# Performance work log

Measured on AMD Instinct MI355X. Metric: run time of the kernel, lower is better.

Reference implementation:

```python
import jax, jax.numpy as jnp
import numpy as np

ALPHA = 1.702
LIMIT = 7.0


def setup_inputs() -> dict:
    key = jax.random.key(0)
    ks = jax.random.split(key, 7)
    B, S, H, D, E, TOPK = 2, 2048, 2048, 2048, 8, 4
    T = B * S
    hidden_states = jax.random.normal(ks[0], (B, S, H), dtype=jnp.float32)
    gate_up_proj = jax.random.normal(ks[1], (E, H, 2 * D), dtype=jnp.float32) * 0.02
    gate_up_proj_bias = jax.random.normal(ks[2], (E, 2 * D), dtype=jnp.float32) * 0.02
    down_proj = jax.random.normal(ks[3], (E, D, H), dtype=jnp.float32) * 0.02
    down_proj_bias = jax.random.normal(ks[4], (E, H), dtype=jnp.float32) * 0.02
    rw = jax.random.uniform(ks[5], (T, E), dtype=jnp.float32)
    routing_weights = rw / jnp.sum(rw, axis=-1, keepdims=True)
    router_indices = jax.random.randint(ks[6], (T, TOPK), 0, E, dtype=jnp.int64)
    return {
        "hidden_states": hidden_states,
        "gate_up_proj": gate_up_proj,
        "gate_up_proj_bias": gate_up_proj_bias,
        "down_proj": down_proj,
        "down_proj_bias": down_proj_bias,
        "routing_weights": routing_weights,
        "router_indices": router_indices,
    }


def geglu(gate_up):
    # interleaved layout: gate = [..., 0::2], up = [..., 1::2]
    gate = gate_up[..., 0::2]
    up = gate_up[..., 1::2]
    gate = jnp.minimum(gate, LIMIT)
    up = jnp.clip(up, -LIMIT, LIMIT)
    glu = gate * jax.nn.sigmoid(gate * ALPHA)
    return (up + 1.0) * glu


def reference(hidden_states, gate_up_proj, gate_up_proj_bias, down_proj,
              down_proj_bias, routing_weights, router_indices):
    B, S, H = hidden_states.shape
    x = hidden_states.reshape(-1, H)  # [T, H]
    # per-expert batched GEMM: [E, T, 2D]
    gate_up = jnp.einsum('th,ehd->etd', x, gate_up_proj) + gate_up_proj_bias[:, None, :]
    act = geglu(gate_up)  # [E, T, D]
    out = jnp.einsum('etd,edh->eth', act, down_proj) + down_proj_bias[:, None, :]
    # weight by router probs and sum over experts
    out = out * routing_weights.T[:, :, None]  # [E, T, H]
    out = jnp.sum(out, axis=0)
    return out.reshape(B, S, H)
```

## Files before the change

### kernel.cpp

```cpp
#include <hip/hip_runtime.h>
#include <hip/hip_bf16.h>

#define ALPHA 1.702f
#define GLIMIT 7.0f

typedef __attribute__((ext_vector_type(4))) float f32x4;
typedef __attribute__((ext_vector_type(8))) __bf16 bf16x8;

typedef __attribute__((address_space(3))) unsigned int as3_uint;
typedef const __attribute__((address_space(1))) unsigned int as1_uint;

__device__ __forceinline__ void async_copy16(void* lds, const void* g) {
    __builtin_amdgcn_global_load_lds((as1_uint*)g, (as3_uint*)lds, 16, 0, 0);
}

__device__ __forceinline__ short f2bf(float f) {
    unsigned u = __float_as_uint(f);
    unsigned r = (u + 0x7fffu + ((u >> 16) & 1u)) >> 16;
    return (short)r;
}

__global__ void cvt_bf16_kernel(const float* __restrict__ src,
                                short* __restrict__ dst, int n4) {
    int i = blockIdx.x * blockDim.x + threadIdx.x;
    if (i < n4) {
        float4 v = reinterpret_cast<const float4*>(src)[i];
        short4 o;
        o.x = f2bf(v.x); o.y = f2bf(v.y); o.z = f2bf(v.z); o.w = f2bf(v.w);
        reinterpret_cast<short4*>(dst)[i] = o;
    }
}

__global__ void transpose_cvt(const float* __restrict__ src,
                              short* __restrict__ dst, int R, int C) {
    __shared__ float t[64][65];
    const int z  = blockIdx.z;
    const int c0 = blockIdx.x * 64;
    const int r0 = blockIdx.y * 64;
    const float* s = src + (size_t)z * R * C;
    short* d = dst + (size_t)z * R * C;
    const int tid = threadIdx.x;
#pragma unroll
    for (int i = 0; i < 16; ++i) {
        int idx = i * 256 + tid;
        int r = idx >> 6, c = idx & 63;
        t[r][c] = s[(size_t)(r0 + r) * C + c0 + c];
    }
    __syncthreads();
#pragma unroll
    for (int i = 0; i < 16; ++i) {
        int idx = i * 256 + tid;
        int r = idx >> 6, c = idx & 63;
        d[(size_t)(c0 + r) * R + r0 + c] = f2bf(t[c][r]);
    }
}


struct Gemm1Src {
    const short* A; const short* B;
    __device__ __forceinline__ const short* operator()(int t, int h) const {
        const short* base = (h & 2) ? B : A;
        return base + ((size_t)(h & 1) << 18) + (size_t)t * 64;
    }
};

struct Gemm2Src {
    const short* act; const short* wdt; size_t aoff, boff; int kh;
    __device__ __forceinline__ const short* operator()(int t, int h) const {
        int g = (kh << 7) + t;
        int e = g >> 5;
        size_t ko = (size_t)(g & 31) << 6;
        if (h & 2) return wdt + ((size_t)e << 22) + boff + ((size_t)(h & 1) << 18) + ko;
        return act + ((size_t)e << 23) + aoff + ((size_t)(h & 1) << 18) + ko;
    }
};

#define PH_BAR()  __builtin_amdgcn_s_barrier()
#define PH_LGKM() do { asm volatile("s_waitcnt lgkmcnt(0)" ::: "memory"); \
                       __builtin_amdgcn_sched_barrier(0); } while (0)

template <typename Src>
__device__ __forceinline__ void gemm_8phase(const Src& src, int NT, char* smem,
                                            f32x4 (&acc)[8][4]) {
    const int tid  = threadIdx.x;
    const int lane = tid & 63;
    const int wid  = tid >> 6;
    const int wr   = wid >> 2;
    const int wcol = wid & 3;
    const int lhi  = lane >> 4;
    const int llo  = lane & 15;

    auto stage = [&](int buf, int h, const short* g) {
        char* dst = smem + buf * 65536 + h * 16384;
        {
            int c = tid, r = c >> 3, s = (c & 7) ^ (r & 7);
            async_copy16(dst + c * 16, g + (size_t)r * 2048 + s * 8);
        }
        {
            int c = tid + 512, r = c >> 3, s = (c & 7) ^ (r & 7);
            async_copy16(dst + c * 16, g + (size_t)r * 2048 + s * 8);
        }
    };
    auto ldfrag = [&](int buf, int h, int row, int slot) {
        return *(const bf16x8*)(smem + buf * 65536 + h * 16384 + row * 128 +
                                ((slot ^ (row & 7)) << 4));
    };

    stage(0, 0, src(0, 0)); stage(0, 2, src(0, 2));
    stage(0, 3, src(0, 3)); stage(0, 1, src(0, 1));
    if (NT > 1) {
        stage(1, 0, src(1, 0)); stage(1, 2, src(1, 2)); stage(1, 3, src(1, 3));
        asm volatile("s_waitcnt vmcnt(6)" ::: "memory");
    } else {
        asm volatile("s_waitcnt vmcnt(0)" ::: "memory");
    }
    PH_BAR();

    bf16x8 a[4][2], b[4][2];
    for (int t = 0; t < NT; ++t) {
        const int cur = t & 1, nxt = cur ^ 1;
#pragma unroll
        for (int m = 0; m < 4; ++m) {
            int row = wr * 64 + m * 16 + llo;
            a[m][0] = ldfrag(cur, 0, row, lhi);
            a[m][1] = ldfrag(cur, 0, row, 4 + lhi);
        }
#pragma unroll
        for (int n = 0; n < 2; ++n) {
            int row = wcol * 32 + n * 16 + llo;
            b[n][0] = ldfrag(cur, 2, row, lhi);
            b[n][1] = ldfrag(cur, 2, row, 4 + lhi);
        }
        if (t + 1 < NT) stage(nxt, 1, src(t + 1, 1));
        PH_BAR(); PH_LGKM();
        __builtin_amdgcn_s_setprio(1);
#pragma unroll
        for (int m = 0; m < 4; ++m)
#pragma unroll
            for (int n = 0; n < 2; ++n)
#pragma unroll
                for (int ks = 0; ks < 2; ++ks)
                    acc[m][n] = __builtin_amdgcn_mfma_f32_16x16x32_bf16(
                        a[m][ks], b[n][ks], acc[m][n], 0, 0, 0);
        __builtin_amdgcn_s_setprio(0);
        PH_BAR();
#pragma unroll
        for (int n = 0; n < 2; ++n) {
            int row = wcol * 32 + n * 16 + llo;
            b[2 + n][0] = ldfrag(cur, 3, row, lhi);
            b[2 + n][1] = ldfrag(cur, 3, row, 4 + lhi);
        }
        if (t + 2 < NT) stage(cur, 0, src(t + 2, 0));
        PH_BAR(); PH_LGKM();
        __builtin_amdgcn_s_setprio(1);
#pragma unroll
        for (int m = 0; m < 4; ++m)
#pragma unroll
            for (int n = 2; n < 4; ++n)
#pragma unroll
                for (int ks = 0; ks < 2; ++ks)
                    acc[m][n] = __builtin_amdgcn_mfma_f32_16x16x32_bf16(
                        a[m][ks], b[n][ks], acc[m][n], 0, 0, 0);
        __builtin_amdgcn_s_setprio(0);
        PH_BAR();
#pragma unroll
        for (int m = 0; m < 4; ++m) {
            int row = wr * 64 + m * 16 + llo;
            a[m][0] = ldfrag(cur, 1, row, lhi);
            a[m][1] = ldfrag(cur, 1, row, 4 + lhi);
        }
        if (t + 2 < NT) stage(cur, 2, src(t + 2, 2));
        PH_BAR(); PH_LGKM();
        __builtin_amdgcn_s_setprio(1);
#pragma unroll
        for (int m = 0; m < 4; ++m)
#pragma unroll
            for (int n = 0; n < 2; ++n)
#pragma unroll
                for (int ks = 0; ks < 2; ++ks)
                    acc[4 + m][n] = __builtin_amdgcn_mfma_f32_16x16x32_bf16(
                        a[m][ks], b[n][ks], acc[4 + m][n], 0, 0, 0);
        __builtin_amdgcn_s_setprio(0);
        PH_BAR();
        if (t + 2 < NT) {
            stage(cur, 3, src(t + 2, 3));
            asm volatile("s_waitcnt vmcnt(6)" ::: "memory");
        } else {
            asm volatile("s_waitcnt vmcnt(0)" ::: "memory");
        }
        PH_BAR();
        __builtin_amdgcn_s_setprio(1);
#pragma unroll
        for (int m = 0; m < 4; ++m)
#pragma unroll
            for (int n = 2; n < 4; ++n)
#pragma unroll
                for (int ks = 0; ks < 2; ++ks)
                    acc[4 + m][n] = __builtin_amdgcn_mfma_f32_16x16x32_bf16(
                        a[m][ks], b[n][ks], acc[4 + m][n], 0, 0, 0);
        __builtin_amdgcn_s_setprio(0);
        PH_BAR();
    }
}

__global__ __launch_bounds__(512, 2) void gemm1_8ph(
    const short* __restrict__ xb, const short* __restrict__ wgut,
    const float* __restrict__ bias, const float* __restrict__ rwp,
    short* __restrict__ act) {
    __shared__ __align__(16) char smem[131072];
    const int e = blockIdx.z;
    int flat = blockIdx.x + (blockIdx.y << 4);
    int swz = (flat & 7) * 32 + (flat >> 3);
    const int n0 = (swz & 15) * 256;
    const int m0 = (swz >> 4) * 256;
    const int tid  = threadIdx.x;
    const int lane = tid & 63;
    const int wid  = tid >> 6;
    const int wr = wid >> 2, wcol = wid & 3;

    f32x4 acc[8][4];
#pragma unroll
    for (int m = 0; m < 8; ++m)
#pragma unroll
        for (int n = 0; n < 4; ++n) acc[m][n] = (f32x4){0.f, 0.f, 0.f, 0.f};

    Gemm1Src src{ xb + (size_t)m0 * 2048,
                  wgut + ((size_t)e << 23) + (size_t)n0 * 2048 };
    gemm_8phase(src, 32, smem, acc);

    __syncthreads();
    float* rws = (float*)smem;
    if (tid < 256) rws[tid] = rwp[(size_t)(m0 + tid) * 8 + e];
    __syncthreads();

    const float* bias_e = bias + (size_t)e * 4096;
    short* acte = act + ((size_t)e << 23);
    const int par = lane & 1;
    float bvn[4];
#pragma unroll
    for (int n = 0; n < 4; ++n) {
        int coln = n0 + (n >> 1) * 128 + wcol * 32 + (n & 1) * 16 + (lane & 15);
        bvn[n] = bias_e[coln];
    }
#pragma unroll
    for (int m = 0; m < 8; ++m) {
        int rowb = (m >> 2) * 128 + wr * 64 + (m & 3) * 16 + ((lane >> 4) << 2);
#pragma unroll
        for (int n = 0; n < 4; ++n) {
            int coln = n0 + (n >> 1) * 128 + wcol * 32 + (n & 1) * 16 + (lane & 15);
            float v[4], o[4];
#pragma unroll
            for (int j = 0; j < 4; ++j) v[j] = acc[m][n][j] + bvn[n];
#pragma unroll
            for (int j = 0; j < 4; ++j) o[j] = __shfl_xor(v[j], 1);
            int dcol = coln >> 1;
#pragma unroll
            for (int jj = 0; jj < 2; ++jj) {
                int j = (par << 1) + jj;
                float g = par ? o[j] : v[j];
                float u = par ? v[j] : o[j];
                g = fminf(g, GLIMIT);
                u = fmaxf(fminf(u, GLIMIT), -GLIMIT);
                float glu = g / (1.f + __expf(-ALPHA * g));
                int row = rowb + j;
                float aa = (u + 1.f) * glu * rws[row];
                acte[(size_t)(m0 + row) * 2048 + dcol] = f2bf(aa);
            }
        }
    }
}

__global__ __launch_bounds__(512, 2) void gemm2_8ph(
    const short* __restrict__ act, const short* __restrict__ wdt,
    float* __restrict__ out, float* __restrict__ part) {
    __shared__ __align__(16) char smem[131072];
    const int kh = blockIdx.z;
    int flat = blockIdx.x + (blockIdx.y << 3);
    int swz = (flat & 7) * 16 + (flat >> 3);
    const int n0 = (swz & 7) * 256;
    const int m0 = (swz >> 3) * 256;
    const int tid  = threadIdx.x;
    const int lane = tid & 63;
    const int wid  = tid >> 6;
    const int wr = wid >> 2, wcol = wid & 3;

    f32x4 acc[8][4];
#pragma unroll
    for (int m = 0; m < 8; ++m)
#pragma unroll
        for (int n = 0; n < 4; ++n) acc[m][n] = (f32x4){0.f, 0.f, 0.f, 0.f};

    Gemm2Src src{ act, wdt, (size_t)m0 * 2048, (size_t)n0 * 2048, kh };
    gemm_8phase(src, 128, smem, acc);

    float* dst = (kh == 0) ? out : part;
#pragma unroll
    for (int m = 0; m < 8; ++m) {
        int row = m0 + (m >> 2) * 128 + wr * 64 + (m & 3) * 16 + ((lane >> 4) << 2);
#pragma unroll
        for (int n = 0; n < 4; ++n) {
            int col = n0 + (n >> 1) * 128 + wcol * 32 + (n & 1) * 16 + (lane & 15);
#pragma unroll
            for (int j = 0; j < 4; ++j)
                dst[(size_t)(row + j) * 2048 + col] = acc[m][n][j];
        }
    }
}

__global__ __launch_bounds__(256) void reduce_bias(
    const float* __restrict__ p1, const float* __restrict__ rw,
    const float* __restrict__ bd, float* __restrict__ out) {
    const int t = blockIdx.x;
    const int tid = threadIdx.x;
    float rwv[8];
#pragma unroll
    for (int e = 0; e < 8; ++e) rwv[e] = rw[(size_t)t * 8 + e];
    size_t base = (size_t)t * 2048;
#pragma unroll
    for (int i = 0; i < 2; ++i) {
        int h = (tid + i * 256) * 4;
        float4 o = *(const float4*)(out + base + h);
        float4 p = *(const float4*)(p1 + base + h);
        o.x += p.x; o.y += p.y; o.z += p.z; o.w += p.w;
#pragma unroll
        for (int e = 0; e < 8; ++e) {
            float4 bb = *(const float4*)(bd + e * 2048 + h);
            o.x += rwv[e] * bb.x; o.y += rwv[e] * bb.y;
            o.z += rwv[e] * bb.z; o.w += rwv[e] * bb.w;
        }
        *(float4*)(out + base + h) = o;
    }
}

extern "C" void kernel_launch(void* const* d_in, const int* in_sizes, int n_in,
                              void* d_out, int out_size, void* d_ws, size_t ws_size,
                              hipStream_t stream) {
    const float* x   = (const float*)d_in[0];
    const float* wgu = (const float*)d_in[1];
    const float* bgu = (const float*)d_in[2];
    const float* wd  = (const float*)d_in[3];
    const float* bd  = (const float*)d_in[4];
    const float* rw  = (const float*)d_in[5];
    float* out = (float*)d_out;

    char* ws = (char*)d_ws;
    short* xb   = (short*)(ws);
    short* wgut = (short*)(ws + 16777216);
    float* p1   = (float*)(ws + 16777216);
    short* wdt  = (short*)(ws + 150994944);
    short* actb = (short*)(ws + 218103808);

    cvt_bf16_kernel<<<8192, 256, 0, stream>>>(x, xb, 2097152);
    transpose_cvt<<<dim3(64, 32, 8), 256, 0, stream>>>(wgu, wgut, 2048, 4096);
    transpose_cvt<<<dim3(32, 32, 8), 256, 0, stream>>>(wd, wdt, 2048, 2048);
    gemm1_8ph<<<dim3(16, 16, 8), 512, 0, stream>>>(xb, wgut, bgu, rw, actb);
    gemm2_8ph<<<dim3(8, 16, 2), 512, 0, stream>>>(actb, wdt, out, p1);
    reduce_bias<<<4096, 256, 0, stream>>>(p1, rw, bd, out);
}
```

Before: 976.9 us.

## Prefetch next-tile B fragments early and stage GEMM1 epilogue through LDS

The 8-phase GEMM loop now loads the first B fragments of the next K-tile at the end of the current iteration, with finer vmcnt waits so each stage only waits for the data it needs. This is meant to hide LDS fragment-load latency behind MFMA work. The GEMM1 epilogue now writes GEGLU outputs into a padded LDS tile and then stores them to global memory as coalesced 16-byte vectors, replacing scattered 2-byte stores. The vmcnt counts are hand-tuned and fragile, and the extra epilogue barrier adds some synchronization.

```diff
diff --git a/kernel.cpp b/kernel.cpp
--- a/kernel.cpp
+++ b/kernel.cpp
@@ -6,6 +6,7 @@
 
 typedef __attribute__((ext_vector_type(4))) float f32x4;
 typedef __attribute__((ext_vector_type(8))) __bf16 bf16x8;
+typedef __attribute__((ext_vector_type(8))) short short8;
 
 typedef __attribute__((address_space(3))) unsigned int as3_uint;
 typedef const __attribute__((address_space(1))) unsigned int as1_uint;
@@ -78,6 +79,7 @@
 #define PH_BAR()  __builtin_amdgcn_s_barrier()
 #define PH_LGKM() do { asm volatile("s_waitcnt lgkmcnt(0)" ::: "memory"); \
                        __builtin_amdgcn_sched_barrier(0); } while (0)
+#define VMW(n)    asm volatile("s_waitcnt vmcnt(" #n ")" ::: "memory")
 
 template <typename Src>
 __device__ __forceinline__ void gemm_8phase(const Src& src, int NT, char* smem,
@@ -108,15 +110,18 @@
 
     stage(0, 0, src(0, 0)); stage(0, 2, src(0, 2));
     stage(0, 3, src(0, 3)); stage(0, 1, src(0, 1));
-    if (NT > 1) {
-        stage(1, 0, src(1, 0)); stage(1, 2, src(1, 2)); stage(1, 3, src(1, 3));
-        asm volatile("s_waitcnt vmcnt(6)" ::: "memory");
-    } else {
-        asm volatile("s_waitcnt vmcnt(0)" ::: "memory");
-    }
+    stage(1, 0, src(1, 0)); stage(1, 2, src(1, 2)); stage(1, 3, src(1, 3));
+    VMW(8);
     PH_BAR();
 
     bf16x8 a[4][2], b[4][2];
+#pragma unroll
+    for (int n = 0; n < 2; ++n) {
+        int row = wcol * 32 + n * 16 + llo;
+        b[n][0] = ldfrag(0, 2, row, lhi);
+        b[n][1] = ldfrag(0, 2, row, 4 + lhi);
+    }
+
     for (int t = 0; t < NT; ++t) {
         const int cur = t & 1, nxt = cur ^ 1;
 #pragma unroll
@@ -124,12 +129,6 @@
             int row = wr * 64 + m * 16 + llo;
             a[m][0] = ldfrag(cur, 0, row, lhi);
             a[m][1] = ldfrag(cur, 0, row, 4 + lhi);
-        }
-#pragma unroll
-        for (int n = 0; n < 2; ++n) {
-            int row = wcol * 32 + n * 16 + llo;
-            b[n][0] = ldfrag(cur, 2, row, lhi);
-            b[n][1] = ldfrag(cur, 2, row, 4 + lhi);
         }
         if (t + 1 < NT) stage(nxt, 1, src(t + 1, 1));
         PH_BAR(); PH_LGKM();
@@ -150,7 +149,9 @@
             b[2 + n][0] = ldfrag(cur, 3, row, lhi);
             b[2 + n][1] = ldfrag(cur, 3, row, 4 + lhi);
         }
-        if (t + 2 < NT) stage(cur, 0, src(t + 2, 0));
+        if (t + 2 < NT) { stage(cur, 0, src(t + 2, 0)); VMW(10); }
+        else if (t + 1 < NT) { VMW(8); }
+        else { VMW(0); }
         PH_BAR(); PH_LGKM();
         __builtin_amdgcn_s_setprio(1);
 #pragma unroll
@@ -182,14 +183,19 @@
                         a[m][ks], b[n][ks], acc[4 + m][n], 0, 0, 0);
         __builtin_amdgcn_s_setprio(0);
         PH_BAR();
-        if (t + 2 < NT) {
-            stage(cur, 3, src(t + 2, 3));
-            asm volatile("s_waitcnt vmcnt(6)" ::: "memory");
-        } else {
-            asm volatile("s_waitcnt vmcnt(0)" ::: "memory");
-        }
-        PH_BAR();
+        if (t + 2 < NT) { stage(cur, 3, src(t + 2, 3)); VMW(8); }
+        else if (t + 1 < NT) { VMW(2); }
+        else { VMW(0); }
+        PH_BAR(); PH_LGKM();
         __builtin_amdgcn_s_setprio(1);
+        if (t + 1 < NT) {
+#pragma unroll
+            for (int n = 0; n < 2; ++n) {
+                int row = wcol * 32 + n * 16 + llo;
+                b[n][0] = ldfrag(nxt, 2, row, lhi);
+                b[n][1] = ldfrag(nxt, 2, row, 4 + lhi);
+            }
+        }
 #pragma unroll
         for (int m = 0; m < 4; ++m)
 #pragma unroll
@@ -217,6 +223,7 @@
     const int lane = tid & 63;
     const int wid  = tid >> 6;
     const int wr = wid >> 2, wcol = wid & 3;
+    const int lhi = lane >> 4, llo = lane & 15;
 
     f32x4 acc[8][4];
 #pragma unroll
@@ -228,32 +235,26 @@
                   wgut + ((size_t)e << 23) + (size_t)n0 * 2048 };
     gemm_8phase(src, 32, smem, acc);
 
-    __syncthreads();
-    float* rws = (float*)smem;
+    short* lact = (short*)smem;
+    float* rws  = (float*)(smem + 69632);
     if (tid < 256) rws[tid] = rwp[(size_t)(m0 + tid) * 8 + e];
     __syncthreads();
 
     const float* bias_e = bias + (size_t)e * 4096;
-    short* acte = act + ((size_t)e << 23);
     const int par = lane & 1;
-    float bvn[4];
 #pragma unroll
     for (int n = 0; n < 4; ++n) {
-        int coln = n0 + (n >> 1) * 128 + wcol * 32 + (n & 1) * 16 + (lane & 15);
-        bvn[n] = bias_e[coln];
-    }
-#pragma unroll
-    for (int m = 0; m < 8; ++m) {
-        int rowb = (m >> 2) * 128 + wr * 64 + (m & 3) * 16 + ((lane >> 4) << 2);
-#pragma unroll
-        for (int n = 0; n < 4; ++n) {
-            int coln = n0 + (n >> 1) * 128 + wcol * 32 + (n & 1) * 16 + (lane & 15);
+        int clocal = (n >> 1) * 128 + wcol * 32 + (n & 1) * 16 + llo;
+        float bv = bias_e[n0 + clocal];
+        int dloc = clocal >> 1;
+#pragma unroll
+        for (int m = 0; m < 8; ++m) {
+            int rowb = (m >> 2) * 128 + wr * 64 + (m & 3) * 16 + (lhi << 2);
             float v[4], o[4];
 #pragma unroll
-            for (int j = 0; j < 4; ++j) v[j] = acc[m][n][j] + bvn[n];
+            for (int j = 0; j < 4; ++j) v[j] = acc[m][n][j] + bv;
 #pragma unroll
             for (int j = 0; j < 4; ++j) o[j] = __shfl_xor(v[j], 1);
-            int dcol = coln >> 1;
 #pragma unroll
             for (int jj = 0; jj < 2; ++jj) {
                 int j = (par << 1) + jj;
@@ -263,10 +264,18 @@
                 u = fmaxf(fminf(u, GLIMIT), -GLIMIT);
                 float glu = g / (1.f + __expf(-ALPHA * g));
                 int row = rowb + j;
-                float aa = (u + 1.f) * glu * rws[row];
-                acte[(size_t)(m0 + row) * 2048 + dcol] = f2bf(aa);
+                lact[row * 136 + dloc] = f2bf((u + 1.f) * glu * rws[row]);
             }
         }
+    }
+    __syncthreads();
+    short* acte = act + ((size_t)e << 23) + (size_t)m0 * 2048 + (n0 >> 1);
+#pragma unroll
+    for (int it = 0; it < 8; ++it) {
+        int idx = it * 512 + tid;
+        int row = idx >> 4, c8 = (idx & 15) << 3;
+        *(short8*)(acte + (size_t)row * 2048 + c8) =
+            *(const short8*)(lact + row * 136 + c8);
     }
 }
 
```

Result: no change. 964.1 us (-1.3%).
